# Performance work log

Measured on AMD Instinct MI355X. Metric: run time of the kernel, lower is better.

## Reference

```python
import jax, jax.numpy as jnp
import numpy as np

WINDOW_SIZE = 11
SIGMA = 1.5
C1 = 0.01 ** 2
C2 = 0.03 ** 2


def _create_window(window_size, channel, dtype):
    coords = jnp.arange(window_size, dtype=jnp.float32) - window_size // 2
    g = jnp.exp(-coords ** 2 / (2.0 * SIGMA ** 2))
    g = g / g.sum()
    win2d = jnp.outer(g, g)  # [k, k]
    # depthwise kernel: [C, 1, k, k] in OIHW with feature_group_count=C
    return jnp.broadcast_to(win2d[None, None], (channel, 1, window_size, window_size)).astype(dtype)


def _dw_conv(x, w, channel):
    pad = WINDOW_SIZE // 2
    return jax.lax.conv_general_dilated(
        x, w,
        window_strides=(1, 1),
        padding=[(pad, pad), (pad, pad)],
        dimension_numbers=('NCHW', 'OIHW', 'NCHW'),
        feature_group_count=channel,
    )


def setup_inputs() -> dict:
    key = jax.random.key(0)
    k1, k2 = jax.random.split(key)
    shape = (16, 3, 512, 512)
    img1 = jax.random.uniform(k1, shape, dtype=jnp.float32)
    img2 = jax.random.uniform(k2, shape, dtype=jnp.float32)
    return {"img1": img1, "img2": img2}


def reference(img1, img2):
    channel = img1.shape[1]
    window = _create_window(WINDOW_SIZE, channel, img1.dtype)

    mu1 = _dw_conv(img1, window, channel)
    mu2 = _dw_conv(img2, window, channel)
    mu1_sq = mu1 * mu1
    mu2_sq = mu2 * mu2
    mu1_mu2 = mu1 * mu2

    sigma1_sq = _dw_conv(img1 * img1, window, channel) - mu1_sq
    sigma2_sq = _dw_conv(img2 * img2, window, channel) - mu2_sq
    sigma12 = _dw_conv(img1 * img2, window, channel) - mu1_mu2

    ssim_map = ((2.0 * mu1_mu2 + C1) * (2.0 * sigma12 + C2)) / (
        (mu1_sq + mu2_sq + C1) * (sigma1_sq + sigma2_sq + C2))
    # forward() returns only the mean SSIM (mcs mean is computed but discarded)
    return ssim_map.mean()
```

## Files before the change

kernel.cpp:

```cpp
#include <hip/hip_runtime.h>
#include <math.h>


#define TX 256
#define TY 34
#define RAD 5
#define KW 11
#define LWP (TX + 2 * RAD)
#define IMG_W 512
#define IMG_H 512
#define C1F 0.0001f
#define C2F 0.0009f

typedef float v2f __attribute__((ext_vector_type(2)));

__global__ __launch_bounds__(256, 5) void ssim_fused_kernel(
    const float* __restrict__ img1,
    const float* __restrict__ img2,
    float* __restrict__ out,
    float inv_n)
{
    __shared__ v2f rows[2][LWP];
    __shared__ float red[4];

    const int tid = threadIdx.x;
    const int x0  = blockIdx.x * TX;
    const int y0  = blockIdx.y * TY;
    const float* __restrict__ p1 = img1 + blockIdx.z * (IMG_W * IMG_H);
    const float* __restrict__ p2 = img2 + blockIdx.z * (IMG_W * IMG_H);

    float g[KW];
    {
        double t[KW];
        double s = 0.0;
        #pragma unroll
        for (int i = 0; i < KW; ++i) {
            const double c = (double)(i - RAD);
            t[i] = exp(-(c * c) / 4.5);
            s += t[i];
        }
        #pragma unroll
        for (int i = 0; i < KW; ++i) {
            const float gi = (float)(t[i] / s);
            g[i] = __int_as_float(__builtin_amdgcn_readfirstlane(__float_as_int(gi)));
        }
    }

    v2f  accMu[KW];
    v2f  accSq[KW];
    float accXy[KW];
    #pragma unroll
    for (int s = 0; s < KW; ++s) {
        accMu[s] = (v2f){0.f, 0.f};
        accSq[s] = (v2f){0.f, 0.f};
        accXy[s] = 0.f;
    }

    float acc = 0.f;

    const int gx0 = x0 - RAD + tid;
    const int gx1 = gx0 + TX;

    #pragma clang loop unroll(disable)
    for (int jb = 0; jb < 4; ++jb) {
        #pragma unroll
        for (int P = 0; P < KW; ++P) {
            const int j  = jb * KW + P;
            const int ir = y0 - RAD + j;
            const int buf = j & 1;
            const bool rowok = ((unsigned)ir < (unsigned)IMG_H);
            const int rb = ir * IMG_W;

            {
                v2f ab = (v2f){0.f, 0.f};
                if (rowok && ((unsigned)gx0 < (unsigned)IMG_W)) {
                    ab.x = p1[rb + gx0];
                    ab.y = p2[rb + gx0];
                }
                rows[buf][tid] = ab;
                if (tid < 2 * RAD) {
                    v2f ab2 = (v2f){0.f, 0.f};
                    if (rowok && ((unsigned)gx1 < (unsigned)IMG_W)) {
                        ab2.x = p1[rb + gx1];
                        ab2.y = p2[rb + gx1];
                    }
                    rows[buf][TX + tid] = ab2;
                }
            }
            __syncthreads();

            v2f hmu = (v2f){0.f, 0.f};
            v2f hsq = (v2f){0.f, 0.f};
            float hxy = 0.f;
            #pragma unroll
            for (int k = 0; k < KW; ++k) {
                const v2f ab = rows[buf][tid + k];
                const v2f w  = g[k] * ab;
                hmu += w;
                hsq = __builtin_elementwise_fma(w, ab, hsq);
                hxy = fmaf(w.x, ab.y, hxy);
            }

            #pragma unroll
            for (int s = 0; s < KW; ++s) {
                const float wt = g[(P - s + KW) % KW];
                const v2f wv = (v2f){wt, wt};
                accMu[s] = __builtin_elementwise_fma(wv, hmu, accMu[s]);
                accSq[s] = __builtin_elementwise_fma(wv, hsq, accSq[s]);
                accXy[s] = fmaf(wt, hxy, accXy[s]);
            }

            const int e  = (P + 1) % KW;
            const int oi = y0 + j - 2 * RAD;
            if (j >= 2 * RAD && oi < IMG_H) {
                const v2f mu   = accMu[e];
                const v2f musq = mu * mu;
                const float mu12 = mu.x * mu.y;
                const v2f sig  = accSq[e] - musq;
                const float s12 = accXy[e] - mu12;
                const float num = (2.f * mu12 + C1F) * (2.f * s12 + C2F);
                const float den = (musq.x + musq.y + C1F) * (sig.x + sig.y + C2F);
                acc += num / den;
            }
            accMu[e] = (v2f){0.f, 0.f};
            accSq[e] = (v2f){0.f, 0.f};
            accXy[e] = 0.f;
        }
    }

    #pragma unroll
    for (int off = 32; off > 0; off >>= 1)
        acc += __shfl_xor(acc, off, 64);
    if ((tid & 63) == 0) red[tid >> 6] = acc;
    __syncthreads();
    if (tid == 0) {
        const float s = red[0] + red[1] + red[2] + red[3];
        atomicAdd(out, s * inv_n);
    }
}

extern "C" void kernel_launch(void* const* d_in, const int* in_sizes, int n_in,
                              void* d_out, int out_size, void* d_ws, size_t ws_size,
                              hipStream_t stream) {
    const float* img1 = (const float*)d_in[0];
    const float* img2 = (const float*)d_in[1];
    float* out = (float*)d_out;

    hipMemsetAsync(out, 0, (size_t)out_size * sizeof(float), stream);

    const float inv_n = 1.0f / (16.0f * 3.0f * 512.0f * 512.0f);
    dim3 grid(IMG_W / TX, (IMG_H + TY - 1) / TY, 16 * 3);
    ssim_fused_kernel<<<grid, dim3(256, 1, 1), 0, stream>>>(img1, img2, out, inv_n);
}
```

Baseline: 171.1 us.

## Split block into wave-private column strips and prefetch next row into registers

```diff
diff --git a/kernel.cpp b/kernel.cpp
--- a/kernel.cpp
+++ b/kernel.cpp
@@ -2,32 +2,37 @@
 #include <math.h>
 
 
-#define TX 256
-#define TY 34
+#define KW 11
 #define RAD 5
-#define KW 11
-#define LWP (TX + 2 * RAD)
 #define IMG_W 512
 #define IMG_H 512
+#define TY 34
+#define NJB 4
+#define LROW 74
 #define C1F 0.0001f
 #define C2F 0.0009f
 
 typedef float v2f __attribute__((ext_vector_type(2)));
 
-__global__ __launch_bounds__(256, 5) void ssim_fused_kernel(
+__global__ __launch_bounds__(256) void ssim_fused_kernel(
     const float* __restrict__ img1,
     const float* __restrict__ img2,
     float* __restrict__ out,
     float inv_n)
 {
-    __shared__ v2f rows[2][LWP];
+    __shared__ v2f rows[4][2][LROW];
     __shared__ float red[4];
 
-    const int tid = threadIdx.x;
-    const int x0  = blockIdx.x * TX;
-    const int y0  = blockIdx.y * TY;
-    const float* __restrict__ p1 = img1 + blockIdx.z * (IMG_W * IMG_H);
-    const float* __restrict__ p2 = img2 + blockIdx.z * (IMG_W * IMG_H);
+    const int tid  = threadIdx.x;
+    const int lane = tid & 63;
+    const int wvi  = tid >> 6;
+
+    const int x0 = (blockIdx.x * 4 + wvi) * 64;
+    const int y0 = blockIdx.y * TY;
+
+    const size_t pbase = (size_t)blockIdx.z * (size_t)(IMG_W * IMG_H);
+    const float* __restrict__ p1 = img1 + pbase;
+    const float* __restrict__ p2 = img2 + pbase;
 
     float g[KW];
     {
@@ -46,8 +51,30 @@
         }
     }
 
-    v2f  accMu[KW];
-    v2f  accSq[KW];
+    const int c0   = x0 - RAD + lane;
+    const int c0c  = min(max(c0, 0), IMG_W - 1);
+    const float m0 = (c0 == c0c) ? 1.f : 0.f;
+    const int c1   = c0 + 64;
+    const int c1c  = min(max(c1, 0), IMG_W - 1);
+    const float m1 = (c1 == c1c) ? 1.f : 0.f;
+
+    auto load_row = [&](int j, v2f& v0, v2f& v1) {
+        const int ir = y0 - RAD + j;
+        v0 = (v2f){0.f, 0.f};
+        v1 = (v2f){0.f, 0.f};
+        if ((unsigned)ir < (unsigned)IMG_H) {
+            const float* r1 = p1 + ir * IMG_W;
+            const float* r2 = p2 + ir * IMG_W;
+            v0.x = r1[c0c] * m0;
+            v0.y = r2[c0c] * m0;
+            if (lane < 2 * RAD) {
+                v1.x = r1[c1c] * m1;
+                v1.y = r2[c1c] * m1;
+            }
+        }
+    };
+
+    v2f  accMu[KW], accSq[KW];
     float accXy[KW];
     #pragma unroll
     for (int s = 0; s < KW; ++s) {
@@ -56,45 +83,31 @@
         accXy[s] = 0.f;
     }
 
+    v2f cur0, cur1;
+    load_row(0, cur0, cur1);
+
     float acc = 0.f;
 
-    const int gx0 = x0 - RAD + tid;
-    const int gx1 = gx0 + TX;
-
     #pragma clang loop unroll(disable)
-    for (int jb = 0; jb < 4; ++jb) {
+    for (int jb = 0; jb < NJB; ++jb) {
         #pragma unroll
         for (int P = 0; P < KW; ++P) {
-            const int j  = jb * KW + P;
-            const int ir = y0 - RAD + j;
+            const int j   = jb * KW + P;
             const int buf = j & 1;
-            const bool rowok = ((unsigned)ir < (unsigned)IMG_H);
-            const int rb = ir * IMG_W;
+            v2f* __restrict__ wrow = rows[wvi][buf];
 
-            {
-                v2f ab = (v2f){0.f, 0.f};
-                if (rowok && ((unsigned)gx0 < (unsigned)IMG_W)) {
-                    ab.x = p1[rb + gx0];
-                    ab.y = p2[rb + gx0];
-                }
-                rows[buf][tid] = ab;
-                if (tid < 2 * RAD) {
-                    v2f ab2 = (v2f){0.f, 0.f};
-                    if (rowok && ((unsigned)gx1 < (unsigned)IMG_W)) {
-                        ab2.x = p1[rb + gx1];
-                        ab2.y = p2[rb + gx1];
-                    }
-                    rows[buf][TX + tid] = ab2;
-                }
-            }
-            __syncthreads();
+            wrow[lane] = cur0;
+            if (lane < 2 * RAD) wrow[64 + lane] = cur1;
+            __threadfence_block();
+
+            load_row(j + 1, cur0, cur1);
 
             v2f hmu = (v2f){0.f, 0.f};
             v2f hsq = (v2f){0.f, 0.f};
             float hxy = 0.f;
             #pragma unroll
             for (int k = 0; k < KW; ++k) {
-                const v2f ab = rows[buf][tid + k];
+                const v2f ab = wrow[lane + k];
                 const v2f w  = g[k] * ab;
                 hmu += w;
                 hsq = __builtin_elementwise_fma(w, ab, hsq);
@@ -104,34 +117,37 @@
             #pragma unroll
             for (int s = 0; s < KW; ++s) {
                 const float wt = g[(P - s + KW) % KW];
-                const v2f wv = (v2f){wt, wt};
-                accMu[s] = __builtin_elementwise_fma(wv, hmu, accMu[s]);
-                accSq[s] = __builtin_elementwise_fma(wv, hsq, accSq[s]);
-                accXy[s] = fmaf(wt, hxy, accXy[s]);
+                const v2f wv2 = (v2f){wt, wt};
+                if (s == P) {
+                    accMu[s] = wv2 * hmu;
+                    accSq[s] = wv2 * hsq;
+                    accXy[s] = wt * hxy;
+                } else {
+                    accMu[s] = __builtin_elementwise_fma(wv2, hmu, accMu[s]);
+                    accSq[s] = __builtin_elementwise_fma(wv2, hsq, accSq[s]);
+                    accXy[s] = fmaf(wt, hxy, accXy[s]);
+                }
             }
 
-            const int e  = (P + 1) % KW;
-            const int oi = y0 + j - 2 * RAD;
-            if (j >= 2 * RAD && oi < IMG_H) {
-                const v2f mu   = accMu[e];
-                const v2f musq = mu * mu;
+            const int oy = y0 + j - 2 * RAD;
+            if (j >= 2 * RAD && oy < IMG_H) {
+                const int e = (P + 1) % KW;
+                const v2f mu    = accMu[e];
+                const v2f musq  = mu * mu;
                 const float mu12 = mu.x * mu.y;
-                const v2f sig  = accSq[e] - musq;
+                const v2f sig   = accSq[e] - musq;
                 const float s12 = accXy[e] - mu12;
-                const float num = (2.f * mu12 + C1F) * (2.f * s12 + C2F);
+                const float num = fmaf(2.f, mu12, C1F) * fmaf(2.f, s12, C2F);
                 const float den = (musq.x + musq.y + C1F) * (sig.x + sig.y + C2F);
-                acc += num / den;
+                acc = fmaf(num, __builtin_amdgcn_rcpf(den), acc);
             }
-            accMu[e] = (v2f){0.f, 0.f};
-            accSq[e] = (v2f){0.f, 0.f};
-            accXy[e] = 0.f;
         }
     }
 
     #pragma unroll
     for (int off = 32; off > 0; off >>= 1)
         acc += __shfl_xor(acc, off, 64);
-    if ((tid & 63) == 0) red[tid >> 6] = acc;
+    if (lane == 0) red[wvi] = acc;
     __syncthreads();
     if (tid == 0) {
         const float s = red[0] + red[1] + red[2] + red[3];
@@ -142,6 +158,7 @@
 extern "C" void kernel_launch(void* const* d_in, const int* in_sizes, int n_in,
                               void* d_out, int out_size, void* d_ws, size_t ws_size,
                               hipStream_t stream) {
+    (void)in_sizes; (void)n_in; (void)d_ws; (void)ws_size;
     const float* img1 = (const float*)d_in[0];
     const float* img2 = (const float*)d_in[1];
     float* out = (float*)d_out;
@@ -149,6 +166,6 @@
     hipMemsetAsync(out, 0, (size_t)out_size * sizeof(float), stream);
 
     const float inv_n = 1.0f / (16.0f * 3.0f * 512.0f * 512.0f);
-    dim3 grid(IMG_W / TX, (IMG_H + TY - 1) / TY, 16 * 3);
+    dim3 grid(2, 16, 16 * 3);
     ssim_fused_kernel<<<grid, dim3(256, 1, 1), 0, stream>>>(img1, img2, out, inv_n);
 }
```

Result: slower. 175.2 us (+2.4%).
